# Kernel tuning notes

Measured on AMD Instinct MI355X. Metric: run time of the kernel, lower is better.

## Reference

```python
import jax, jax.numpy as jnp
import numpy as np

THRESHOLD = 1.0   # threshold_value
ALPHA = 2.0       # spikingjelly surrogate.ATan default alpha


@jax.custom_vjp
def spike(x):
    # Heaviside forward, ATan surrogate backward
    return (x >= 0.0).astype(x.dtype)

def _spike_fwd(x):
    return spike(x), x

def _spike_bwd(x, g):
    # d/dx [ (1/pi) * atan(pi/2 * alpha * x) + 1/2 ] = (alpha/2) / (1 + (pi/2*alpha*x)^2)
    return (g * (ALPHA / 2.0) / (1.0 + (jnp.pi / 2.0 * ALPHA * x) ** 2),)

spike.defvjp(_spike_fwd, _spike_bwd)


def _if_node(v, inp):
    # IFNode with v_reset=None (soft/residual reset): v += I; s = H(v - th); v -= s*th
    v = v + inp
    s = spike(v - THRESHOLD)
    v = v - s * THRESHOLD
    return v, s


def setup_inputs() -> dict:
    key = jax.random.key(0)
    ks = jax.random.split(key, 7)
    B, T = 1024, 128
    H1, H2, C = 512, 256, 18
    def lin(k, fan_out, fan_in):
        bound = 1.0 / np.sqrt(fan_in)
        kw, kb = jax.random.split(k)
        W = jax.random.uniform(kw, (fan_out, fan_in), jnp.float32, -bound, bound)
        b = jax.random.uniform(kb, (fan_out,), jnp.float32, -bound, bound)
        return W, b
    W1, b1 = lin(ks[0], H1, 1)
    W2, b2 = lin(ks[1], H2, H1)
    W3, b3 = lin(ks[2], C, H2)
    x = jax.random.normal(ks[3], (B, T), jnp.float32)
    return {"x": x, "W1": W1, "b1": b1, "W2": W2, "b2": b2,
            "W3": W3, "b3": b3, "repeat": 1}


def reference(x, W1, b1, W2, b2, W3, b3, repeat):
    B, T = x.shape
    H1, H2, C = W1.shape[0], W2.shape[0], W3.shape[0]

    def step(carry, xt):
        v1, v2, v3, acc = carry
        out = xt[:, None]                       # [B, 1]
        for _ in range(repeat):                  # original code only valid for repeat == 1
            v1, s1 = _if_node(v1, out @ W1.T + b1)   # [B, H1]
            v2, s2 = _if_node(v2, s1 @ W2.T + b2)    # [B, H2]
            v3, s3 = _if_node(v3, s2 @ W3.T + b3)    # [B, C]
            out = s3
        return (v1, v2, v3, acc + out), None

    z = lambda d: jnp.zeros((B, d), x.dtype)
    init = (z(H1), z(H2), z(C), z(C))
    (_, _, _, acc), _ = jax.lax.scan(step, init, x.T)   # scan over T timesteps
    return acc / T
```

## Files before the change

### kernel.cpp

```cpp
#include <hip/hip_runtime.h>
#include <cmath>

#define BB  1024
#define TT  128
#define HH1 512
#define HH2 256
#define CC  18

#define WS_DIG   0ull
#define WS_W3D   524288ull
#define WS_MASK  557056ull
#define WS_MASK2 8945664ull
#define WS_D3    13139968ull

typedef int  v4i  __attribute__((ext_vector_type(4)));
typedef int  v16i __attribute__((ext_vector_type(16)));
typedef unsigned long long ull;

__device__ __forceinline__ v4i expand_bits(unsigned bits) {
  v4i a;
  a.x = (int)((( bits        & 15u) * 0x204081u) & 0x01010101u);
  a.y = (int)((((bits >>  4) & 15u) * 0x204081u) & 0x01010101u);
  a.z = (int)((((bits >>  8) & 15u) * 0x204081u) & 0x01010101u);
  a.w = (int)((((bits >> 12) & 15u) * 0x204081u) & 0x01010101u);
  return a;
}

__global__ __launch_bounds__(256) void prep_weights(const float* __restrict__ W2,
    const float* __restrict__ W3, signed char* __restrict__ dig,
    signed char* __restrict__ w3dig)
{
  const int bid = blockIdx.x, tid = threadIdx.x;
  if (bid < 2048) {
    int i = bid * 256 + tid;
    int j = i & 15, n = (i >> 4) & 31, h = (i >> 9) & 1;
    int s = (i >> 10) & 15, d = (i >> 14) & 3, st = i >> 16;
    int h1 = s * 32 + h * 16 + j;
    int h2 = st * 32 + n;
    float w = W2[h2 * HH1 + h1];
    long long ll = llrint((double)w * 4294967296.0);
    int v = (int)ll;
    signed char d0 = (signed char)(v & 255); v = (v - d0) >> 8;
    signed char d1 = (signed char)(v & 255); v = (v - d1) >> 8;
    signed char d2 = (signed char)(v & 255); v = (v - d2) >> 8;
    signed char d3 = (signed char)v;
    dig[i] = (d == 0) ? d0 : (d == 1) ? d1 : (d == 2) ? d2 : d3;
  } else {
    int i = (bid - 2048) * 256 + tid;
    int j = i & 15, col = (i >> 4) & 31, h = (i >> 9) & 1;
    int c8 = (i >> 10) & 7, d = (i >> 13) & 3;
    int h2 = c8 * 32 + h * 16 + j;
    float w = (col < CC) ? W3[col * HH2 + h2] : 0.0f;
    long long ll = llrint((double)w * 4294967296.0);
    int v = (int)ll;
    signed char d0 = (signed char)(v & 255); v = (v - d0) >> 8;
    signed char d1 = (signed char)(v & 255); v = (v - d1) >> 8;
    signed char d2 = (signed char)(v & 255); v = (v - d2) >> 8;
    signed char d3 = (signed char)v;
    w3dig[i] = (d == 0) ? d0 : (d == 1) ? d1 : (d == 2) ? d2 : d3;
  }
}

__global__ __launch_bounds__(256) void phase_s1(const float* __restrict__ x,
    const float* __restrict__ W1, const float* __restrict__ b1,
    ull* __restrict__ masks)
{
  __shared__ float xrow[TT];
  int row = blockIdx.x, tid = threadIdx.x, wv = tid >> 6, lane = tid & 63;
  for (int i = tid; i < TT; i += 256) xrow[i] = x[row * TT + i];
  const float w1a = W1[tid], w1b = W1[tid + 256];
  const float b1a = b1[tid], b1b = b1[tid + 256];
  float v1a = 0.f, v1b = 0.f;
  __syncthreads();
  for (int t = 0; t < TT; ++t) {
    float xt = xrow[t];
    float iA = __fadd_rn(__fmul_rn(xt, w1a), b1a);
    v1a = __fadd_rn(v1a, iA);
    bool sA = (v1a >= 1.0f);  v1a = sA ? (v1a - 1.0f) : v1a;
    float iB = __fadd_rn(__fmul_rn(xt, w1b), b1b);
    v1b = __fadd_rn(v1b, iB);
    bool sB = (v1b >= 1.0f);  v1b = sB ? (v1b - 1.0f) : v1b;
    ull mA = __ballot(sA);
    ull mB = __ballot(sB);
    if (lane == 0) {
      ull* p = masks + (size_t)row * 1024 + (size_t)(t >> 5) * 256 + (t & 31);
      p[(size_t)wv * 32]       = mA;
      p[(size_t)(4 + wv) * 32] = mB;
    }
  }
}

__global__ __launch_bounds__(512, 2) void phase_gemmscan(
    const signed char* __restrict__ Bd, const ull* __restrict__ masks,
    const float* __restrict__ b2, unsigned* __restrict__ masks2)
{
  __shared__ __align__(16) signed char Bl[65536];
  __shared__ __align__(16) ull mbuf[16][128];

  const int bid = blockIdx.x;
  const int rowgrp = bid & 31, stripe = bid >> 5;
  const int tid = threadIdx.x, lane = tid & 63, wv = tid >> 6;
  const int half = lane >> 5, l31 = lane & 31;

  {
    const uint4* src = (const uint4*)(Bd + (size_t)stripe * 65536);
    uint4* dst = (uint4*)Bl;
#pragma unroll
    for (int i = 0; i < 8; ++i) dst[tid + 512 * i] = src[tid + 512 * i];
  }

  const signed char* bbase = Bl + half * 512 + l31 * 16;
  const float b2r = b2[stripe * 32 + l31];
  const unsigned hsh = half * 16;

  const int tp1 = (l31 & 3) + ((l31 >> 3) << 2) + ((l31 & 4) ? 16 : 0);
  const int tp2 = tp1 ^ 16;

  __syncthreads();

  if (wv & 4) {
    __builtin_amdgcn_s_sleep(15);
    __builtin_amdgcn_s_sleep(15);
  }

  for (int tau = 0; tau < 2; ++tau) {
    const int pr = wv + 8 * tau;
    const int r1 = rowgrp * 32 + 2 * pr;
    const ull* mb1 = masks + (size_t)r1 * 1024;
    const ull* mb2 = mb1 + 1024;
    float v2 = 0.f;

    ull wP[8], wQ[8], wPn[8], wQn[8];
#pragma unroll
    for (int k = 0; k < 8; ++k) {
      wP[k] = mb1[k * 32 + tp1];
      wQ[k] = mb2[k * 32 + tp2];
    }

#pragma unroll
    for (int c = 0; c < 4; ++c) {
      if (c < 3) {
#pragma unroll
        for (int k = 0; k < 8; ++k) {
          wPn[k] = mb1[(c + 1) * 256 + k * 32 + tp1];
          wQn[k] = mb2[(c + 1) * 256 + k * 32 + tp2];
        }
      }

      v16i aP[4], aQ[4];
#pragma unroll
      for (int d = 0; d < 4; ++d) {
        aP[d] = (v16i){0,0,0,0,0,0,0,0,0,0,0,0,0,0,0,0};
        aQ[d] = (v16i){0,0,0,0,0,0,0,0,0,0,0,0,0,0,0,0};
      }
      __builtin_amdgcn_s_setprio(1);
#pragma unroll
      for (int s = 0; s < 16; ++s) {
        v4i q0 = *(const v4i*)(bbase + (0 * 16 + s) * 1024);
        v4i q1 = *(const v4i*)(bbase + (1 * 16 + s) * 1024);
        v4i q2 = *(const v4i*)(bbase + (2 * 16 + s) * 1024);
        v4i q3 = *(const v4i*)(bbase + (3 * 16 + s) * 1024);
        unsigned shift = ((s & 1) << 5) + hsh;
        v4i eP = expand_bits((unsigned)(wP[s >> 1] >> shift) & 0xFFFFu);
        v4i eQ = expand_bits((unsigned)(wQ[s >> 1] >> shift) & 0xFFFFu);
        aP[0] = __builtin_amdgcn_mfma_i32_32x32x32_i8(eP, q0, aP[0], 0, 0, 0);
        aQ[0] = __builtin_amdgcn_mfma_i32_32x32x32_i8(eQ, q0, aQ[0], 0, 0, 0);
        aP[1] = __builtin_amdgcn_mfma_i32_32x32x32_i8(eP, q1, aP[1], 0, 0, 0);
        aQ[1] = __builtin_amdgcn_mfma_i32_32x32x32_i8(eQ, q1, aQ[1], 0, 0, 0);
        aP[2] = __builtin_amdgcn_mfma_i32_32x32x32_i8(eP, q2, aP[2], 0, 0, 0);
        aQ[2] = __builtin_amdgcn_mfma_i32_32x32x32_i8(eQ, q2, aQ[2], 0, 0, 0);
        aP[3] = __builtin_amdgcn_mfma_i32_32x32x32_i8(eP, q3, aP[3], 0, 0, 0);
        aQ[3] = __builtin_amdgcn_mfma_i32_32x32x32_i8(eQ, q3, aQ[3], 0, 0, 0);
      }
      __builtin_amdgcn_s_setprio(0);

      float dP[16], dQ[16];
#pragma unroll
      for (int r = 0; r < 16; ++r) {
        int sloP = aP[0][r] + (aP[1][r] << 8);
        int shiP = aP[2][r] + (aP[3][r] << 8);
        double ssP = fma((double)shiP, 65536.0, (double)sloP);
        dP[r] = (float)(ssP * 0x1p-32);
        int sloQ = aQ[0][r] + (aQ[1][r] << 8);
        int shiQ = aQ[2][r] + (aQ[3][r] << 8);
        double ssQ = fma((double)shiQ, 65536.0, (double)sloQ);
        dQ[r] = (float)(ssQ * 0x1p-32);
      }

      const int tb = c * 32;
#pragma unroll
      for (int r = 0; r < 16; ++r) {
        float val = half ? dQ[r] : dP[r];
        float i2 = __fadd_rn(val, b2r);
        v2 = __fadd_rn(v2, i2);
        bool s2 = (v2 >= 1.0f);  v2 = s2 ? (v2 - 1.0f) : v2;
        ull m = __ballot(s2);
        if (lane == 0) mbuf[pr][tb + r] = m;
      }
      v2 = __shfl_xor(v2, 32);
#pragma unroll
      for (int r = 0; r < 16; ++r) {
        float val = half ? dP[r] : dQ[r];
        float i2 = __fadd_rn(val, b2r);
        v2 = __fadd_rn(v2, i2);
        bool s2 = (v2 >= 1.0f);  v2 = s2 ? (v2 - 1.0f) : v2;
        ull m = __ballot(s2);
        if (lane == 0) mbuf[pr][tb + 16 + r] = (m >> 32) | (m << 32);
      }
      v2 = __shfl_xor(v2, 32);

      if (c < 3) {
#pragma unroll
        for (int k = 0; k < 8; ++k) { wP[k] = wPn[k]; wQ[k] = wQn[k]; }
      }
    }
  }

  __syncthreads();
  {
    const ull* mb = &mbuf[0][0];
    unsigned* base = masks2 + (size_t)rowgrp * 32 * 1024 + stripe;
#pragma unroll
    for (int i = 0; i < 4; ++i) {
      int e = i * 512 + tid;
      int p = e >> 7, t = e & 127;
      ull m = mb[e];
      unsigned* q = base + (size_t)(2 * p) * 1024 + t * 8;
      q[0]    = (unsigned)m;
      q[1024] = (unsigned)(m >> 32);
    }
  }
}

__global__ __launch_bounds__(256) void phase_l3v3(const signed char* __restrict__ W3d,
    const unsigned* __restrict__ masks2, const float* __restrict__ b3,
    float* __restrict__ out)
{
  __shared__ __align__(16) signed char Bl[32768];
  const int bid = blockIdx.x;
  const int tid = threadIdx.x, lane = tid & 63, wv = tid >> 6;
  const int half = lane >> 5, l31 = lane & 31;

  {
    const uint4* src = (const uint4*)W3d;
    uint4* dst = (uint4*)Bl;
#pragma unroll
    for (int i = 0; i < 8; ++i) dst[tid + 256 * i] = src[tid + 256 * i];
  }

  const int row = bid * 4 + wv;
  const unsigned* mrow = masks2 + (size_t)row * (TT * 8);
  const signed char* bbase = Bl + half * 512 + l31 * 16;
  const float b3r = b3[l31 < CC ? l31 : 0];
  const unsigned hsh = half * 16;
  const int tp1 = (l31 & 3) + ((l31 >> 3) << 2) + ((l31 & 4) ? 16 : 0);

  __syncthreads();

  float v3 = 0.f, ac = 0.f;

  for (int c = 0; c < 4; ++c) {
    unsigned w8[8];
    {
      const unsigned* mp = mrow + (size_t)(c * 32 + tp1) * 8;
      *(uint4*)&w8[0] = *(const uint4*)mp;
      *(uint4*)&w8[4] = *(const uint4*)(mp + 4);
    }

    v16i acc[4];
#pragma unroll
    for (int d = 0; d < 4; ++d)
      acc[d] = (v16i){0,0,0,0,0,0,0,0,0,0,0,0,0,0,0,0};

#pragma unroll
    for (int c8 = 0; c8 < 8; ++c8) {
      v4i e = expand_bits((w8[c8] >> hsh) & 0xFFFFu);
#pragma unroll
      for (int d = 0; d < 4; ++d) {
        v4i b = *(const v4i*)(bbase + (d * 8 + c8) * 1024);
        acc[d] = __builtin_amdgcn_mfma_i32_32x32x32_i8(e, b, acc[d], 0, 0, 0);
      }
    }

    float dv[16];
#pragma unroll
    for (int r = 0; r < 16; ++r) {
      int slo = acc[0][r] + (acc[1][r] << 8);
      int shi = acc[2][r] + (acc[3][r] << 8);
      double ss = fma((double)shi, 65536.0, (double)slo);
      dv[r] = (float)(ss * 0x1p-32);
    }

#pragma unroll
    for (int r = 0; r < 16; ++r) {
      float i3 = __fadd_rn(dv[r], b3r);
      float u  = __fadd_rn(v3, i3);
      bool s3  = (u >= 1.0f);
      float uv = s3 ? (u - 1.0f) : u;
      float av = __fadd_rn(ac, s3 ? 1.0f : 0.0f);
      if (!half) { v3 = uv; ac = av; }
    }
    v3 = __shfl_xor(v3, 32); ac = __shfl_xor(ac, 32);
#pragma unroll
    for (int r = 0; r < 16; ++r) {
      float i3 = __fadd_rn(dv[r], b3r);
      float u  = __fadd_rn(v3, i3);
      bool s3  = (u >= 1.0f);
      float uv = s3 ? (u - 1.0f) : u;
      float av = __fadd_rn(ac, s3 ? 1.0f : 0.0f);
      if (half) { v3 = uv; ac = av; }
    }
    v3 = __shfl_xor(v3, 32); ac = __shfl_xor(ac, 32);
  }

  if (!half && l31 < CC)
    out[row * CC + l31] = ac * (1.0f / TT);
}

extern "C" void kernel_launch(void* const* d_in, const int* in_sizes, int n_in,
                              void* d_out, int out_size, void* d_ws, size_t ws_size,
                              hipStream_t stream)
{
  (void)in_sizes; (void)n_in; (void)out_size; (void)ws_size;
  const float* x  = (const float*)d_in[0];
  const float* W1 = (const float*)d_in[1];
  const float* b1 = (const float*)d_in[2];
  const float* W2 = (const float*)d_in[3];
  const float* b2 = (const float*)d_in[4];
  const float* W3 = (const float*)d_in[5];
  const float* b3 = (const float*)d_in[6];
  float* out = (float*)d_out;
  char*  ws  = (char*)d_ws;

  signed char* dig    = (signed char*)(ws + WS_DIG);
  signed char* w3dig  = (signed char*)(ws + WS_W3D);
  ull*         masks  = (ull*)(ws + WS_MASK);
  unsigned*    masks2 = (unsigned*)(ws + WS_MASK2);

  prep_weights<<<2176, 256, 0, stream>>>(W2, W3, dig, w3dig);
  phase_s1<<<1024, 256, 0, stream>>>(x, W1, b1, masks);
  phase_gemmscan<<<256, 512, 0, stream>>>(dig, masks, b2, masks2);
  phase_l3v3<<<256, 256, 0, stream>>>(w3dig, masks2, b3, out);
}
```

Measured before the change: 172.2 us.

## Fuse four phase kernels into one cooperative kernel with grid syncs

Merges weight digit prep, layer-1 spike scan, the layer-2 int8 MFMA GEMM-scan and the layer-3 stage into a single cooperative kernel of 256 blocks of 512 threads, with grid-wide syncs between phases. This removes three kernel launch boundaries and their gaps. The cost is that the early phases now run on 256 blocks instead of 1024 to 2176, layer-1 rows are processed two passes per block, and half the waves sit idle during the layer-3 phase. Grid sync adds its own overhead.

```diff
diff --git a/kernel.cpp b/kernel.cpp
--- a/kernel.cpp
+++ b/kernel.cpp
@@ -1,5 +1,8 @@
 #include <hip/hip_runtime.h>
+#include <hip/hip_cooperative_groups.h>
 #include <cmath>
+
+namespace cg = cooperative_groups;
 
 #define BB  1024
 #define TT  128
@@ -11,7 +14,6 @@
 #define WS_W3D   524288ull
 #define WS_MASK  557056ull
 #define WS_MASK2 8945664ull
-#define WS_D3    13139968ull
 
 typedef int  v4i  __attribute__((ext_vector_type(4)));
 typedef int  v16i __attribute__((ext_vector_type(16)));
@@ -26,295 +28,297 @@
   return a;
 }
 
-__global__ __launch_bounds__(256) void prep_weights(const float* __restrict__ W2,
-    const float* __restrict__ W3, signed char* __restrict__ dig,
-    signed char* __restrict__ w3dig)
-{
-  const int bid = blockIdx.x, tid = threadIdx.x;
-  if (bid < 2048) {
-    int i = bid * 256 + tid;
-    int j = i & 15, n = (i >> 4) & 31, h = (i >> 9) & 1;
-    int s = (i >> 10) & 15, d = (i >> 14) & 3, st = i >> 16;
-    int h1 = s * 32 + h * 16 + j;
-    int h2 = st * 32 + n;
-    float w = W2[h2 * HH1 + h1];
-    long long ll = llrint((double)w * 4294967296.0);
-    int v = (int)ll;
-    signed char d0 = (signed char)(v & 255); v = (v - d0) >> 8;
-    signed char d1 = (signed char)(v & 255); v = (v - d1) >> 8;
-    signed char d2 = (signed char)(v & 255); v = (v - d2) >> 8;
-    signed char d3 = (signed char)v;
-    dig[i] = (d == 0) ? d0 : (d == 1) ? d1 : (d == 2) ? d2 : d3;
-  } else {
-    int i = (bid - 2048) * 256 + tid;
-    int j = i & 15, col = (i >> 4) & 31, h = (i >> 9) & 1;
-    int c8 = (i >> 10) & 7, d = (i >> 13) & 3;
-    int h2 = c8 * 32 + h * 16 + j;
-    float w = (col < CC) ? W3[col * HH2 + h2] : 0.0f;
-    long long ll = llrint((double)w * 4294967296.0);
-    int v = (int)ll;
-    signed char d0 = (signed char)(v & 255); v = (v - d0) >> 8;
-    signed char d1 = (signed char)(v & 255); v = (v - d1) >> 8;
-    signed char d2 = (signed char)(v & 255); v = (v - d2) >> 8;
-    signed char d3 = (signed char)v;
-    w3dig[i] = (d == 0) ? d0 : (d == 1) ? d1 : (d == 2) ? d2 : d3;
-  }
+__device__ __forceinline__ signed char dig_of(float w, int d) {
+  long long ll = llrint((double)w * 4294967296.0);
+  int v = (int)ll;
+  signed char d0 = (signed char)(v & 255); v = (v - d0) >> 8;
+  signed char d1 = (signed char)(v & 255); v = (v - d1) >> 8;
+  signed char d2 = (signed char)(v & 255); v = (v - d2) >> 8;
+  signed char d3 = (signed char)v;
+  return (d == 0) ? d0 : (d == 1) ? d1 : (d == 2) ? d2 : d3;
 }
 
-__global__ __launch_bounds__(256) void phase_s1(const float* __restrict__ x,
-    const float* __restrict__ W1, const float* __restrict__ b1,
-    ull* __restrict__ masks)
-{
-  __shared__ float xrow[TT];
-  int row = blockIdx.x, tid = threadIdx.x, wv = tid >> 6, lane = tid & 63;
-  for (int i = tid; i < TT; i += 256) xrow[i] = x[row * TT + i];
-  const float w1a = W1[tid], w1b = W1[tid + 256];
-  const float b1a = b1[tid], b1b = b1[tid + 256];
-  float v1a = 0.f, v1b = 0.f;
-  __syncthreads();
-  for (int t = 0; t < TT; ++t) {
-    float xt = xrow[t];
-    float iA = __fadd_rn(__fmul_rn(xt, w1a), b1a);
-    v1a = __fadd_rn(v1a, iA);
-    bool sA = (v1a >= 1.0f);  v1a = sA ? (v1a - 1.0f) : v1a;
-    float iB = __fadd_rn(__fmul_rn(xt, w1b), b1b);
-    v1b = __fadd_rn(v1b, iB);
-    bool sB = (v1b >= 1.0f);  v1b = sB ? (v1b - 1.0f) : v1b;
-    ull mA = __ballot(sA);
-    ull mB = __ballot(sB);
-    if (lane == 0) {
-      ull* p = masks + (size_t)row * 1024 + (size_t)(t >> 5) * 256 + (t & 31);
-      p[(size_t)wv * 32]       = mA;
-      p[(size_t)(4 + wv) * 32] = mB;
-    }
-  }
-}
-
-__global__ __launch_bounds__(512, 2) void phase_gemmscan(
-    const signed char* __restrict__ Bd, const ull* __restrict__ masks,
-    const float* __restrict__ b2, unsigned* __restrict__ masks2)
+__global__ __launch_bounds__(512, 2) void mega(
+    const float* __restrict__ x,  const float* __restrict__ W1,
+    const float* __restrict__ b1, const float* __restrict__ W2,
+    const float* __restrict__ b2, const float* __restrict__ W3,
+    const float* __restrict__ b3, signed char* __restrict__ dig,
+    signed char* __restrict__ w3dig, ull* __restrict__ masks,
+    unsigned* __restrict__ masks2, float* __restrict__ out)
 {
   __shared__ __align__(16) signed char Bl[65536];
   __shared__ __align__(16) ull mbuf[16][128];
 
-  const int bid = blockIdx.x;
-  const int rowgrp = bid & 31, stripe = bid >> 5;
-  const int tid = threadIdx.x, lane = tid & 63, wv = tid >> 6;
-  const int half = lane >> 5, l31 = lane & 31;
-
-  {
-    const uint4* src = (const uint4*)(Bd + (size_t)stripe * 65536);
-    uint4* dst = (uint4*)Bl;
-#pragma unroll
-    for (int i = 0; i < 8; ++i) dst[tid + 512 * i] = src[tid + 512 * i];
-  }
-
-  const signed char* bbase = Bl + half * 512 + l31 * 16;
-  const float b2r = b2[stripe * 32 + l31];
-  const unsigned hsh = half * 16;
-
-  const int tp1 = (l31 & 3) + ((l31 >> 3) << 2) + ((l31 & 4) ? 16 : 0);
-  const int tp2 = tp1 ^ 16;
-
-  __syncthreads();
-
-  if (wv & 4) {
-    __builtin_amdgcn_s_sleep(15);
-    __builtin_amdgcn_s_sleep(15);
-  }
-
-  for (int tau = 0; tau < 2; ++tau) {
-    const int pr = wv + 8 * tau;
-    const int r1 = rowgrp * 32 + 2 * pr;
-    const ull* mb1 = masks + (size_t)r1 * 1024;
-    const ull* mb2 = mb1 + 1024;
-    float v2 = 0.f;
-
-    ull wP[8], wQ[8], wPn[8], wQn[8];
-#pragma unroll
-    for (int k = 0; k < 8; ++k) {
-      wP[k] = mb1[k * 32 + tp1];
-      wQ[k] = mb2[k * 32 + tp2];
-    }
-
-#pragma unroll
-    for (int c = 0; c < 4; ++c) {
-      if (c < 3) {
-#pragma unroll
-        for (int k = 0; k < 8; ++k) {
-          wPn[k] = mb1[(c + 1) * 256 + k * 32 + tp1];
-          wQn[k] = mb2[(c + 1) * 256 + k * 32 + tp2];
-        }
-      }
-
-      v16i aP[4], aQ[4];
-#pragma unroll
-      for (int d = 0; d < 4; ++d) {
-        aP[d] = (v16i){0,0,0,0,0,0,0,0,0,0,0,0,0,0,0,0};
-        aQ[d] = (v16i){0,0,0,0,0,0,0,0,0,0,0,0,0,0,0,0};
-      }
-      __builtin_amdgcn_s_setprio(1);
-#pragma unroll
-      for (int s = 0; s < 16; ++s) {
-        v4i q0 = *(const v4i*)(bbase + (0 * 16 + s) * 1024);
-        v4i q1 = *(const v4i*)(bbase + (1 * 16 + s) * 1024);
-        v4i q2 = *(const v4i*)(bbase + (2 * 16 + s) * 1024);
-        v4i q3 = *(const v4i*)(bbase + (3 * 16 + s) * 1024);
-        unsigned shift = ((s & 1) << 5) + hsh;
-        v4i eP = expand_bits((unsigned)(wP[s >> 1] >> shift) & 0xFFFFu);
-        v4i eQ = expand_bits((unsigned)(wQ[s >> 1] >> shift) & 0xFFFFu);
-        aP[0] = __builtin_amdgcn_mfma_i32_32x32x32_i8(eP, q0, aP[0], 0, 0, 0);
-        aQ[0] = __builtin_amdgcn_mfma_i32_32x32x32_i8(eQ, q0, aQ[0], 0, 0, 0);
-        aP[1] = __builtin_amdgcn_mfma_i32_32x32x32_i8(eP, q1, aP[1], 0, 0, 0);
-        aQ[1] = __builtin_amdgcn_mfma_i32_32x32x32_i8(eQ, q1, aQ[1], 0, 0, 0);
-        aP[2] = __builtin_amdgcn_mfma_i32_32x32x32_i8(eP, q2, aP[2], 0, 0, 0);
-        aQ[2] = __builtin_amdgcn_mfma_i32_32x32x32_i8(eQ, q2, aQ[2], 0, 0, 0);
-        aP[3] = __builtin_amdgcn_mfma_i32_32x32x32_i8(eP, q3, aP[3], 0, 0, 0);
-        aQ[3] = __builtin_amdgcn_mfma_i32_32x32x32_i8(eQ, q3, aQ[3], 0, 0, 0);
-      }
-      __builtin_amdgcn_s_setprio(0);
-
-      float dP[16], dQ[16];
-#pragma unroll
-      for (int r = 0; r < 16; ++r) {
-        int sloP = aP[0][r] + (aP[1][r] << 8);
-        int shiP = aP[2][r] + (aP[3][r] << 8);
-        double ssP = fma((double)shiP, 65536.0, (double)sloP);
-        dP[r] = (float)(ssP * 0x1p-32);
-        int sloQ = aQ[0][r] + (aQ[1][r] << 8);
-        int shiQ = aQ[2][r] + (aQ[3][r] << 8);
-        double ssQ = fma((double)shiQ, 65536.0, (double)sloQ);
-        dQ[r] = (float)(ssQ * 0x1p-32);
-      }
-
-      const int tb = c * 32;
-#pragma unroll
-      for (int r = 0; r < 16; ++r) {
-        float val = half ? dQ[r] : dP[r];
-        float i2 = __fadd_rn(val, b2r);
-        v2 = __fadd_rn(v2, i2);
-        bool s2 = (v2 >= 1.0f);  v2 = s2 ? (v2 - 1.0f) : v2;
-        ull m = __ballot(s2);
-        if (lane == 0) mbuf[pr][tb + r] = m;
-      }
-      v2 = __shfl_xor(v2, 32);
-#pragma unroll
-      for (int r = 0; r < 16; ++r) {
-        float val = half ? dP[r] : dQ[r];
-        float i2 = __fadd_rn(val, b2r);
-        v2 = __fadd_rn(v2, i2);
-        bool s2 = (v2 >= 1.0f);  v2 = s2 ? (v2 - 1.0f) : v2;
-        ull m = __ballot(s2);
-        if (lane == 0) mbuf[pr][tb + 16 + r] = (m >> 32) | (m << 32);
-      }
-      v2 = __shfl_xor(v2, 32);
-
-      if (c < 3) {
-#pragma unroll
-        for (int k = 0; k < 8; ++k) { wP[k] = wPn[k]; wQ[k] = wQn[k]; }
-      }
-    }
-  }
-
-  __syncthreads();
-  {
-    const ull* mb = &mbuf[0][0];
-    unsigned* base = masks2 + (size_t)rowgrp * 32 * 1024 + stripe;
-#pragma unroll
-    for (int i = 0; i < 4; ++i) {
-      int e = i * 512 + tid;
-      int p = e >> 7, t = e & 127;
-      ull m = mb[e];
-      unsigned* q = base + (size_t)(2 * p) * 1024 + t * 8;
-      q[0]    = (unsigned)m;
-      q[1024] = (unsigned)(m >> 32);
-    }
-  }
-}
-
-__global__ __launch_bounds__(256) void phase_l3v3(const signed char* __restrict__ W3d,
-    const unsigned* __restrict__ masks2, const float* __restrict__ b3,
-    float* __restrict__ out)
-{
-  __shared__ __align__(16) signed char Bl[32768];
+  cg::grid_group grid = cg::this_grid();
   const int bid = blockIdx.x;
   const int tid = threadIdx.x, lane = tid & 63, wv = tid >> 6;
   const int half = lane >> 5, l31 = lane & 31;
 
   {
-    const uint4* src = (const uint4*)W3d;
-    uint4* dst = (uint4*)Bl;
-#pragma unroll
-    for (int i = 0; i < 8; ++i) dst[tid + 256 * i] = src[tid + 256 * i];
+    const int g = bid * 512 + tid;
+#pragma unroll
+    for (int p = 0; p < 4; ++p) {
+      int i = g + p * 131072;
+      int j = i & 15, n = (i >> 4) & 31, h = (i >> 9) & 1;
+      int s = (i >> 10) & 15, d = (i >> 14) & 3, st = i >> 16;
+      dig[i] = dig_of(W2[(st * 32 + n) * HH1 + (s * 32 + h * 16 + j)], d);
+    }
+    if (g < 32768) {
+      int i = g;
+      int j = i & 15, col = (i >> 4) & 31, h = (i >> 9) & 1;
+      int c8 = (i >> 10) & 7, d = (i >> 13) & 3;
+      float w = (col < CC) ? W3[col * HH2 + (c8 * 32 + h * 16 + j)] : 0.0f;
+      w3dig[i] = dig_of(w, d);
+    }
   }
 
-  const int row = bid * 4 + wv;
-  const unsigned* mrow = masks2 + (size_t)row * (TT * 8);
-  const signed char* bbase = Bl + half * 512 + l31 * 16;
-  const float b3r = b3[l31 < CC ? l31 : 0];
-  const unsigned hsh = half * 16;
-  const int tp1 = (l31 & 3) + ((l31 >> 3) << 2) + ((l31 & 4) ? 16 : 0);
-
-  __syncthreads();
-
-  float v3 = 0.f, ac = 0.f;
-
-  for (int c = 0; c < 4; ++c) {
-    unsigned w8[8];
+  {
+    float* xr = (float*)mbuf;
+    const int grp = tid >> 8, t256 = tid & 255;
+    const int wv4 = t256 >> 6;
+    const float w1a = W1[t256], w1b = W1[t256 + 256];
+    const float b1a = b1[t256], b1b = b1[t256 + 256];
+#pragma unroll
+    for (int p = 0; p < 2; ++p) {
+      const int row = p * 512 + bid * 2 + grp;
+      if (t256 < TT) xr[grp * TT + t256] = x[row * TT + t256];
+      __syncthreads();
+      float v1a = 0.f, v1b = 0.f;
+      ull* mp = masks + (size_t)row * 1024;
+      for (int t = 0; t < TT; ++t) {
+        float xt = xr[grp * TT + t];
+        float iA = __fadd_rn(__fmul_rn(xt, w1a), b1a);
+        v1a = __fadd_rn(v1a, iA);
+        bool sA = (v1a >= 1.0f);  v1a = sA ? (v1a - 1.0f) : v1a;
+        float iB = __fadd_rn(__fmul_rn(xt, w1b), b1b);
+        v1b = __fadd_rn(v1b, iB);
+        bool sB = (v1b >= 1.0f);  v1b = sB ? (v1b - 1.0f) : v1b;
+        ull mA = __ballot(sA);
+        ull mB = __ballot(sB);
+        if (lane == 0) {
+          ull* q = mp + (size_t)(t >> 5) * 256 + (t & 31);
+          q[(size_t)wv4 * 32]       = mA;
+          q[(size_t)(4 + wv4) * 32] = mB;
+        }
+      }
+      __syncthreads();
+    }
+  }
+
+  __threadfence();
+  grid.sync();
+
+  {
+    const int rowgrp = bid & 31, stripe = bid >> 5;
     {
-      const unsigned* mp = mrow + (size_t)(c * 32 + tp1) * 8;
-      *(uint4*)&w8[0] = *(const uint4*)mp;
-      *(uint4*)&w8[4] = *(const uint4*)(mp + 4);
-    }
-
-    v16i acc[4];
-#pragma unroll
-    for (int d = 0; d < 4; ++d)
-      acc[d] = (v16i){0,0,0,0,0,0,0,0,0,0,0,0,0,0,0,0};
-
-#pragma unroll
-    for (int c8 = 0; c8 < 8; ++c8) {
-      v4i e = expand_bits((w8[c8] >> hsh) & 0xFFFFu);
-#pragma unroll
-      for (int d = 0; d < 4; ++d) {
-        v4i b = *(const v4i*)(bbase + (d * 8 + c8) * 1024);
-        acc[d] = __builtin_amdgcn_mfma_i32_32x32x32_i8(e, b, acc[d], 0, 0, 0);
-      }
-    }
-
-    float dv[16];
-#pragma unroll
-    for (int r = 0; r < 16; ++r) {
-      int slo = acc[0][r] + (acc[1][r] << 8);
-      int shi = acc[2][r] + (acc[3][r] << 8);
-      double ss = fma((double)shi, 65536.0, (double)slo);
-      dv[r] = (float)(ss * 0x1p-32);
-    }
-
-#pragma unroll
-    for (int r = 0; r < 16; ++r) {
-      float i3 = __fadd_rn(dv[r], b3r);
-      float u  = __fadd_rn(v3, i3);
-      bool s3  = (u >= 1.0f);
-      float uv = s3 ? (u - 1.0f) : u;
-      float av = __fadd_rn(ac, s3 ? 1.0f : 0.0f);
-      if (!half) { v3 = uv; ac = av; }
-    }
-    v3 = __shfl_xor(v3, 32); ac = __shfl_xor(ac, 32);
-#pragma unroll
-    for (int r = 0; r < 16; ++r) {
-      float i3 = __fadd_rn(dv[r], b3r);
-      float u  = __fadd_rn(v3, i3);
-      bool s3  = (u >= 1.0f);
-      float uv = s3 ? (u - 1.0f) : u;
-      float av = __fadd_rn(ac, s3 ? 1.0f : 0.0f);
-      if (half) { v3 = uv; ac = av; }
-    }
-    v3 = __shfl_xor(v3, 32); ac = __shfl_xor(ac, 32);
+      const uint4* src = (const uint4*)(dig + (size_t)stripe * 65536);
+      uint4* dst = (uint4*)Bl;
+#pragma unroll
+      for (int i = 0; i < 8; ++i) dst[tid + 512 * i] = src[tid + 512 * i];
+    }
+
+    const signed char* bbase = Bl + half * 512 + l31 * 16;
+    const float b2r = b2[stripe * 32 + l31];
+    const unsigned hsh = half * 16;
+    const int tp1 = (l31 & 3) + ((l31 >> 3) << 2) + ((l31 & 4) ? 16 : 0);
+    const int tp2 = tp1 ^ 16;
+
+    __syncthreads();
+
+    if (wv & 4) {
+      __builtin_amdgcn_s_sleep(15);
+      __builtin_amdgcn_s_sleep(15);
+    }
+
+    for (int tau = 0; tau < 2; ++tau) {
+      const int pr = wv + 8 * tau;
+      const int r1 = rowgrp * 32 + 2 * pr;
+      const ull* mb1 = masks + (size_t)r1 * 1024;
+      const ull* mb2 = mb1 + 1024;
+      float v2 = 0.f;
+
+      ull wP[8], wQ[8], wPn[8], wQn[8];
+#pragma unroll
+      for (int k = 0; k < 8; ++k) {
+        wP[k] = mb1[k * 32 + tp1];
+        wQ[k] = mb2[k * 32 + tp2];
+      }
+
+#pragma unroll
+      for (int c = 0; c < 4; ++c) {
+        if (c < 3) {
+#pragma unroll
+          for (int k = 0; k < 8; ++k) {
+            wPn[k] = mb1[(c + 1) * 256 + k * 32 + tp1];
+            wQn[k] = mb2[(c + 1) * 256 + k * 32 + tp2];
+          }
+        }
+
+        v16i aP[4], aQ[4];
+#pragma unroll
+        for (int d = 0; d < 4; ++d) {
+          aP[d] = (v16i){0,0,0,0,0,0,0,0,0,0,0,0,0,0,0,0};
+          aQ[d] = (v16i){0,0,0,0,0,0,0,0,0,0,0,0,0,0,0,0};
+        }
+        __builtin_amdgcn_s_setprio(1);
+#pragma unroll
+        for (int s = 0; s < 16; ++s) {
+          v4i q0 = *(const v4i*)(bbase + (0 * 16 + s) * 1024);
+          v4i q1 = *(const v4i*)(bbase + (1 * 16 + s) * 1024);
+          v4i q2 = *(const v4i*)(bbase + (2 * 16 + s) * 1024);
+          v4i q3 = *(const v4i*)(bbase + (3 * 16 + s) * 1024);
+          unsigned shift = ((s & 1) << 5) + hsh;
+          v4i eP = expand_bits((unsigned)(wP[s >> 1] >> shift) & 0xFFFFu);
+          v4i eQ = expand_bits((unsigned)(wQ[s >> 1] >> shift) & 0xFFFFu);
+          aP[0] = __builtin_amdgcn_mfma_i32_32x32x32_i8(eP, q0, aP[0], 0, 0, 0);
+          aQ[0] = __builtin_amdgcn_mfma_i32_32x32x32_i8(eQ, q0, aQ[0], 0, 0, 0);
+          aP[1] = __builtin_amdgcn_mfma_i32_32x32x32_i8(eP, q1, aP[1], 0, 0, 0);
+          aQ[1] = __builtin_amdgcn_mfma_i32_32x32x32_i8(eQ, q1, aQ[1], 0, 0, 0);
+          aP[2] = __builtin_amdgcn_mfma_i32_32x32x32_i8(eP, q2, aP[2], 0, 0, 0);
+          aQ[2] = __builtin_amdgcn_mfma_i32_32x32x32_i8(eQ, q2, aQ[2], 0, 0, 0);
+          aP[3] = __builtin_amdgcn_mfma_i32_32x32x32_i8(eP, q3, aP[3], 0, 0, 0);
+          aQ[3] = __builtin_amdgcn_mfma_i32_32x32x32_i8(eQ, q3, aQ[3], 0, 0, 0);
+        }
+        __builtin_amdgcn_s_setprio(0);
+
+        float dP[16], dQ[16];
+#pragma unroll
+        for (int r = 0; r < 16; ++r) {
+          int sloP = aP[0][r] + (aP[1][r] << 8);
+          int shiP = aP[2][r] + (aP[3][r] << 8);
+          double ssP = fma((double)shiP, 65536.0, (double)sloP);
+          dP[r] = (float)(ssP * 0x1p-32);
+          int sloQ = aQ[0][r] + (aQ[1][r] << 8);
+          int shiQ = aQ[2][r] + (aQ[3][r] << 8);
+          double ssQ = fma((double)shiQ, 65536.0, (double)sloQ);
+          dQ[r] = (float)(ssQ * 0x1p-32);
+        }
+
+        const int tb = c * 32;
+#pragma unroll
+        for (int r = 0; r < 16; ++r) {
+          float val = half ? dQ[r] : dP[r];
+          float i2 = __fadd_rn(val, b2r);
+          v2 = __fadd_rn(v2, i2);
+          bool s2 = (v2 >= 1.0f);  v2 = s2 ? (v2 - 1.0f) : v2;
+          ull m = __ballot(s2);
+          if (lane == 0) mbuf[pr][tb + r] = m;
+        }
+        v2 = __shfl_xor(v2, 32);
+#pragma unroll
+        for (int r = 0; r < 16; ++r) {
+          float val = half ? dP[r] : dQ[r];
+          float i2 = __fadd_rn(val, b2r);
+          v2 = __fadd_rn(v2, i2);
+          bool s2 = (v2 >= 1.0f);  v2 = s2 ? (v2 - 1.0f) : v2;
+          ull m = __ballot(s2);
+          if (lane == 0) mbuf[pr][tb + 16 + r] = (m >> 32) | (m << 32);
+        }
+        v2 = __shfl_xor(v2, 32);
+
+        if (c < 3) {
+#pragma unroll
+          for (int k = 0; k < 8; ++k) { wP[k] = wPn[k]; wQ[k] = wQn[k]; }
+        }
+      }
+    }
+
+    __syncthreads();
+    {
+      const ull* mb = &mbuf[0][0];
+      unsigned* base = masks2 + (size_t)rowgrp * 32 * 1024 + stripe;
+#pragma unroll
+      for (int i = 0; i < 4; ++i) {
+        int e = i * 512 + tid;
+        int p = e >> 7, t = e & 127;
+        ull m = mb[e];
+        unsigned* q = base + (size_t)(2 * p) * 1024 + t * 8;
+        q[0]    = (unsigned)m;
+        q[1024] = (unsigned)(m >> 32);
+      }
+    }
   }
 
-  if (!half && l31 < CC)
-    out[row * CC + l31] = ac * (1.0f / TT);
+  __threadfence();
+  grid.sync();
+
+  {
+    {
+      const uint4* src = (const uint4*)w3dig;
+      uint4* dst = (uint4*)Bl;
+#pragma unroll
+      for (int i = 0; i < 4; ++i) dst[tid + 512 * i] = src[tid + 512 * i];
+    }
+    __syncthreads();
+
+    if (wv < 4) {
+      const int row = bid * 4 + wv;
+      const unsigned* mrow = masks2 + (size_t)row * (TT * 8);
+      const signed char* bbase = Bl + half * 512 + l31 * 16;
+      const float b3r = b3[l31 < CC ? l31 : 0];
+      const unsigned hsh = half * 16;
+      const int tp1 = (l31 & 3) + ((l31 >> 3) << 2) + ((l31 & 4) ? 16 : 0);
+
+      float v3 = 0.f, ac = 0.f;
+
+      for (int c = 0; c < 4; ++c) {
+        unsigned w8[8];
+        {
+          const unsigned* mp = mrow + (size_t)(c * 32 + tp1) * 8;
+          *(uint4*)&w8[0] = *(const uint4*)mp;
+          *(uint4*)&w8[4] = *(const uint4*)(mp + 4);
+        }
+
+        v16i acc[4];
+#pragma unroll
+        for (int d = 0; d < 4; ++d)
+          acc[d] = (v16i){0,0,0,0,0,0,0,0,0,0,0,0,0,0,0,0};
+
+#pragma unroll
+        for (int c8 = 0; c8 < 8; ++c8) {
+          v4i e = expand_bits((w8[c8] >> hsh) & 0xFFFFu);
+#pragma unroll
+          for (int d = 0; d < 4; ++d) {
+            v4i b = *(const v4i*)(bbase + (d * 8 + c8) * 1024);
+            acc[d] = __builtin_amdgcn_mfma_i32_32x32x32_i8(e, b, acc[d], 0, 0, 0);
+          }
+        }
+
+        float dv[16];
+#pragma unroll
+        for (int r = 0; r < 16; ++r) {
+          int slo = acc[0][r] + (acc[1][r] << 8);
+          int shi = acc[2][r] + (acc[3][r] << 8);
+          double ss = fma((double)shi, 65536.0, (double)slo);
+          dv[r] = (float)(ss * 0x1p-32);
+        }
+
+#pragma unroll
+        for (int r = 0; r < 16; ++r) {
+          float i3 = __fadd_rn(dv[r], b3r);
+          float u  = __fadd_rn(v3, i3);
+          bool s3  = (u >= 1.0f);
+          float uv = s3 ? (u - 1.0f) : u;
+          float av = __fadd_rn(ac, s3 ? 1.0f : 0.0f);
+          if (!half) { v3 = uv; ac = av; }
+        }
+        v3 = __shfl_xor(v3, 32); ac = __shfl_xor(ac, 32);
+#pragma unroll
+        for (int r = 0; r < 16; ++r) {
+          float i3 = __fadd_rn(dv[r], b3r);
+          float u  = __fadd_rn(v3, i3);
+          bool s3  = (u >= 1.0f);
+          float uv = s3 ? (u - 1.0f) : u;
+          float av = __fadd_rn(ac, s3 ? 1.0f : 0.0f);
+          if (half) { v3 = uv; ac = av; }
+        }
+        v3 = __shfl_xor(v3, 32); ac = __shfl_xor(ac, 32);
+      }
+
+      if (!half && l31 < CC)
+        out[row * CC + l31] = ac * (1.0f / TT);
+    }
+  }
 }
 
 extern "C" void kernel_launch(void* const* d_in, const int* in_sizes, int n_in,
@@ -337,8 +341,9 @@
   ull*         masks  = (ull*)(ws + WS_MASK);
   unsigned*    masks2 = (unsigned*)(ws + WS_MASK2);
 
-  prep_weights<<<2176, 256, 0, stream>>>(W2, W3, dig, w3dig);
-  phase_s1<<<1024, 256, 0, stream>>>(x, W1, b1, masks);
-  phase_gemmscan<<<256, 512, 0, stream>>>(dig, masks, b2, masks2);
-  phase_l3v3<<<256, 256, 0, stream>>>(w3dig, masks2, b3, out);
+  void* args[] = { (void*)&x, (void*)&W1, (void*)&b1, (void*)&W2, (void*)&b2,
+                   (void*)&W3, (void*)&b3, (void*)&dig, (void*)&w3dig,
+                   (void*)&masks, (void*)&masks2, (void*)&out };
+  hipLaunchCooperativeKernel((const void*)mega, dim3(256), dim3(512),
+                             args, 0, stream);
 }
```

Result: slower. 356.3 us (+106.9%).
